# Kernel tuning notes

Hardware: AMD Instinct MI355X
Metric: run time of the kernel (lower is better)

Reference implementation:

```python
import jax, jax.numpy as jnp
import numpy as np

NEG_INF = -1e9


def setup_inputs() -> dict:
    key = jax.random.key(0)
    k1, k2, k3, k4, k5, k6 = jax.random.split(key, 6)
    B, P, N, C, H = 32, 512, 64, 9, 128
    polylines = jax.random.normal(k1, (B, P, N, C), dtype=jnp.float32)
    polylines_mask = jax.random.uniform(k2, (B, P, N)) > 0.1
    # MLP params (Linear(C,H) -> ReLU -> Linear(H,H)), torch-style init scale
    W1 = jax.random.uniform(k3, (C, H), minval=-1.0, maxval=1.0) / jnp.sqrt(C)
    b1 = jax.random.uniform(k4, (H,), minval=-1.0, maxval=1.0) / jnp.sqrt(C)
    W2 = jax.random.uniform(k5, (H, H), minval=-1.0, maxval=1.0) / jnp.sqrt(H)
    b2 = jax.random.uniform(k6, (H,), minval=-1.0, maxval=1.0) / jnp.sqrt(H)
    return {"polylines": polylines, "polylines_mask": polylines_mask,
            "W1": W1, "b1": b1, "W2": W2, "b2": b2}


def reference(polylines, polylines_mask, W1, b1, W2, b2):
    # Point MLP applied to all points (invalid ones are overwritten below,
    # identical math to the torch masked-gather version).
    h = jax.nn.relu(jnp.einsum('bpnc,ch->bpnh', polylines, W1) + b1)
    feat = jnp.einsum('bpnh,hd->bpnd', h, W2) + b2  # [B,P,N,H]
    feat = jnp.where(polylines_mask[..., None], feat, NEG_INF)
    pooled = jnp.max(feat, axis=2)  # [B,P,H]
    # Polylines with no valid points pooled to NEG_INF -> zero them out.
    any_valid = jnp.any(polylines_mask, axis=2)  # [B,P]
    return jnp.where(any_valid[..., None], pooled, 0.0)
```

## Files before the change

### kernel.cpp

```cpp
#include <hip/hip_runtime.h>


using bf16x8 = __attribute__((ext_vector_type(8))) short;
using f32x4  = __attribute__((ext_vector_type(4))) float;

#define MFMA32(A,B,C) __builtin_amdgcn_mfma_f32_16x16x32_bf16((A),(B),(C),0,0,0)

__device__ __forceinline__ unsigned short f2bf(float f) {
  union { float f; unsigned int u; } v; v.f = f;
  unsigned int r = v.u + 0x7fffu + ((v.u >> 16) & 1u);
  return (unsigned short)(r >> 16);
}

__device__ __forceinline__ unsigned int pack_bf2(float a, float b) {
  union { float f; unsigned int u; } ua, ub; ua.f = a; ub.f = b;
  return __builtin_amdgcn_perm(ub.u + 0x8000u, ua.u + 0x8000u, 0x07060302u);
}

__global__ void prep1(const float* __restrict__ W1, const float* __restrict__ W2,
                      const void* __restrict__ mask,
                      unsigned short* __restrict__ w1sw, unsigned short* __restrict__ w2sw,
                      int* __restrict__ flag) {
  int b = blockIdx.x, t = threadIdx.x;
  if (b == 0) {
    __shared__ int cnt;
    if (t == 0) cnt = 0;
    __syncthreads();
    const unsigned char* mb = (const unsigned char*)mask;
    int local = 0;
    for (int i = t * 16; i < t * 16 + 16; i++) local += (mb[i] != 0) ? 1 : 0;
    atomicAdd(&cnt, local);
    __syncthreads();
    if (t == 0) *flag = (cnt > 2800) ? 1 : 0;
  } else if (b <= 2) {
    int e = (b - 1) * 256 + t;
    int lane = e & 63, grp = e >> 6;
    int li = lane & 15, q = lane >> 4;
    int h = grp * 16 + li;
    int c0 = q * 8;
    #pragma unroll
    for (int j = 0; j < 8; j++) {
      int c = c0 + j;
      w1sw[e * 8 + j] = f2bf((c < 9) ? W1[c * 128 + h] : 0.f);
    }
  } else {
    int e = (b - 3) * 256 + t;
    if (e < 2048) {
      int lane = e & 63, grp = e >> 6;
      int wr = grp >> 4, sub = grp & 15;
      int ks = sub >> 2, td = sub & 3;
      int li = lane & 15, q = lane >> 4;
      int d = wr * 64 + td * 16 + li;
      int h0 = ks * 32 + q * 8;
      #pragma unroll
      for (int j = 0; j < 8; j++)
        w2sw[e * 8 + j] = f2bf(W2[(h0 + j) * 128 + d]);
    }
  }
}

__global__ void prep2(const void* __restrict__ mask, const int* __restrict__ flagp,
                      unsigned long long* __restrict__ bits) {
  int gid = blockIdx.x * 256 + threadIdx.x;
  int flag = *flagp;
  bool v;
  if (flag) v = ((const unsigned char*)mask)[gid] != 0;
  else      v = ((const int*)mask)[gid] != 0;
  unsigned long long bm = __ballot(v);
  if ((threadIdx.x & 63) == 0)
    bits[blockIdx.x * 4 + (threadIdx.x >> 6)] = bm;
}

__global__ __launch_bounds__(256, 4) void poly_main_k(
    const float* __restrict__ X, const void* __restrict__ mask,
    const float* __restrict__ b1g, const float* __restrict__ b2g,
    const unsigned short* __restrict__ w1sw, const unsigned short* __restrict__ w2sw,
    const int* __restrict__ flagp, const unsigned long long* __restrict__ bits,
    int use_bits, float* __restrict__ out)
{
  __shared__ __align__(16) float Xs[1152];
  __shared__ __align__(16) unsigned short Hb[128 * 136];

  const int tid  = threadIdx.x;
  const int lane = tid & 63;
  const int w    = tid >> 6;
  const int wr   = w >> 1, wc = w & 1;
  const int li   = lane & 15, q = lane >> 4;

  float mf[4];
  if (use_bits) {
    unsigned long long bm = bits[(long long)blockIdx.x * 2 + wc];
    #pragma unroll
    for (int tm = 0; tm < 4; tm++)
      mf[tm] = ((bm >> (tm * 16 + li)) & 1ull) ? 0.f : -4e9f;
  } else {
    int flag = *flagp;
    long long mb = (long long)blockIdx.x * 128 + wc * 64 + li;
    if (flag) {
      const unsigned char* mp = (const unsigned char*)mask;
      #pragma unroll
      for (int tm = 0; tm < 4; tm++) mf[tm] = mp[mb + tm * 16] ? 0.f : -4e9f;
    } else {
      const int* mp = (const int*)mask;
      #pragma unroll
      for (int tm = 0; tm < 4; tm++) mf[tm] = mp[mb + tm * 16] ? 0.f : -4e9f;
    }
  }

  {
    const f32x4* xg = (const f32x4*)(X + (long long)blockIdx.x * 1152);
    f32x4* xl = (f32x4*)Xs;
    xl[tid] = xg[tid];
    if (tid < 32) xl[tid + 256] = xg[tid + 256];
  }
  __syncthreads();

  bf16x8 bx[4];
  #pragma unroll
  for (int tm = 0; tm < 4; tm++) {
    int m = wc * 64 + tm * 16 + li;
    const float* xr = Xs + m * 9;
    union { bf16x8 v; unsigned int u[4]; } uu;
    uu.u[0] = uu.u[1] = uu.u[2] = uu.u[3] = 0u;
    if (q == 0) {
      uu.u[0] = pack_bf2(xr[0], xr[1]); uu.u[1] = pack_bf2(xr[2], xr[3]);
      uu.u[2] = pack_bf2(xr[4], xr[5]); uu.u[3] = pack_bf2(xr[6], xr[7]);
    } else if (q == 1) {
      uu.u[0] = pack_bf2(xr[8], 0.f);
    }
    bx[tm] = uu.v;
  }

  f32x4 acc1[4][4];
  #pragma unroll
  for (int a = 0; a < 4; a++)
    #pragma unroll
    for (int b = 0; b < 4; b++) acc1[a][b] = f32x4{0.f, 0.f, 0.f, 0.f};
  {
    bf16x8 a1[4];
    #pragma unroll
    for (int th = 0; th < 4; th++)
      a1[th] = *(const bf16x8*)(w1sw + ((wr * 4 + th) * 64 + lane) * 8);
    #pragma unroll
    for (int th = 0; th < 4; th++)
      #pragma unroll
      for (int tm = 0; tm < 4; tm++)
        acc1[th][tm] = MFMA32(a1[th], bx[tm], acc1[th][tm]);
  }

  #pragma unroll
  for (int th = 0; th < 4; th++) {
    f32x4 bv = *(const f32x4*)(b1g + wr * 64 + th * 16 + q * 4);
    #pragma unroll
    for (int tm = 0; tm < 4; tm++) {
      int m = wc * 64 + tm * 16 + li;
      float v0 = fmaxf(acc1[th][tm][0] + bv[0], 0.f);
      float v1 = fmaxf(acc1[th][tm][1] + bv[1], 0.f);
      float v2 = fmaxf(acc1[th][tm][2] + bv[2], 0.f);
      float v3 = fmaxf(acc1[th][tm][3] + bv[3], 0.f);
      uint2 hv;
      hv.x = pack_bf2(v0, v1);
      hv.y = pack_bf2(v2, v3);
      *(uint2*)(Hb + m * 136 + wr * 64 + th * 16 + q * 4) = hv;
    }
  }
  __syncthreads();

  f32x4 acc2[4][4];
  #pragma unroll
  for (int a = 0; a < 4; a++)
    #pragma unroll
    for (int b = 0; b < 4; b++) acc2[a][b] = f32x4{0.f, 0.f, 0.f, 0.f};
  #pragma unroll
  for (int ks = 0; ks < 4; ks++) {
    bf16x8 a2[4], bb[4];
    #pragma unroll
    for (int td = 0; td < 4; td++)
      a2[td] = *(const bf16x8*)(w2sw + (((wr * 16 + ks * 4 + td) * 64) + lane) * 8);
    #pragma unroll
    for (int tm = 0; tm < 4; tm++)
      bb[tm] = *(const bf16x8*)(Hb + (wc * 64 + tm * 16 + li) * 136 + ks * 32 + q * 8);
    #pragma unroll
    for (int td = 0; td < 4; td++)
      #pragma unroll
      for (int tm = 0; tm < 4; tm++)
        acc2[td][tm] = MFMA32(a2[td], bb[tm], acc2[td][tm]);
  }

  f32x4 pooled[4];
  #pragma unroll
  for (int td = 0; td < 4; td++) {
    f32x4 bv = *(const f32x4*)(b2g + wr * 64 + td * 16 + q * 4);
    #pragma unroll
    for (int r = 0; r < 4; r++) {
      float v0 = acc2[td][0][r] + mf[0];
      float v1 = acc2[td][1][r] + mf[1];
      float v2 = acc2[td][2][r] + mf[2];
      float v3 = acc2[td][3][r] + mf[3];
      pooled[td][r] = fmaxf(fmaxf(v0, v1), fmaxf(v2, v3)) + bv[r];
    }
  }

  __syncthreads();
  float* P = (float*)Hb;
  #pragma unroll
  for (int td = 0; td < 4; td++)
    *(f32x4*)(P + (wc * 16 + li) * 132 + wr * 64 + td * 16 + q * 4) = pooled[td];
  __syncthreads();

  {
    int p = tid >> 7, d = tid & 127;
    const float* Pp = P + p * (16 * 132) + d;
    float v = Pp[0];
    #pragma unroll
    for (int j = 1; j < 16; j++) v = fmaxf(v, Pp[j * 132]);
    if (v < -1e8f) v = 0.f;
    out[(long long)blockIdx.x * 256 + tid] = v;
  }
}

extern "C" void kernel_launch(void* const* d_in, const int* in_sizes, int n_in,
                              void* d_out, int out_size, void* d_ws, size_t ws_size,
                              hipStream_t stream) {
  const float* X    = (const float*)d_in[0];
  const void*  mask = d_in[1];
  const float* W1   = (const float*)d_in[2];
  const float* b1   = (const float*)d_in[3];
  const float* W2   = (const float*)d_in[4];
  const float* b2   = (const float*)d_in[5];
  float* out = (float*)d_out;

  unsigned short* w1sw = (unsigned short*)d_ws;
  unsigned short* w2sw = (unsigned short*)((char*)d_ws + 8192);
  int* flag            = (int*)((char*)d_ws + 40960);
  unsigned long long* bits = (unsigned long long*)((char*)d_ws + 49152);
  int use_bits = (ws_size >= (size_t)(49152 + 131072)) ? 1 : 0;

  prep1<<<11, 256, 0, stream>>>(W1, W2, mask, w1sw, w2sw, flag);
  if (use_bits) prep2<<<4096, 256, 0, stream>>>(mask, flag, bits);
  poly_main_k<<<8192, 256, 0, stream>>>(X, mask, b1, b2, w1sw, w2sw, flag, bits,
                                        use_bits, out);
}
```

Baseline: 143.1 us.

## Alias shared buffers, swizzle H tile, fold biases into accumulators, drop mask prepass

Xs, the hidden tile and the pooling buffer now share one 32KB LDS region, and the launch-bound occupancy target goes from 4 to 5 blocks. The hidden tile drops its padded stride in favour of an XOR-swizzled layout to avoid bank conflicts. Both biases now seed the MFMA accumulators, removing separate add passes, and the max reductions are vectorised. The separate mask-bitmask kernel is removed, so the main kernel reads the mask directly, saving a launch but making per-lane mask loads. The extra sync and aliasing add ordering constraints.

```diff
diff --git a/kernel.cpp b/kernel.cpp
--- a/kernel.cpp
+++ b/kernel.cpp
@@ -5,6 +5,10 @@
 using f32x4  = __attribute__((ext_vector_type(4))) float;
 
 #define MFMA32(A,B,C) __builtin_amdgcn_mfma_f32_16x16x32_bf16((A),(B),(C),0,0,0)
+
+__device__ __forceinline__ f32x4 vmax4(f32x4 a, f32x4 b) {
+  return __builtin_elementwise_max(a, b);
+}
 
 __device__ __forceinline__ unsigned short f2bf(float f) {
   union { float f; unsigned int u; } v; v.f = f;
@@ -59,27 +63,16 @@
   }
 }
 
-__global__ void prep2(const void* __restrict__ mask, const int* __restrict__ flagp,
-                      unsigned long long* __restrict__ bits) {
-  int gid = blockIdx.x * 256 + threadIdx.x;
-  int flag = *flagp;
-  bool v;
-  if (flag) v = ((const unsigned char*)mask)[gid] != 0;
-  else      v = ((const int*)mask)[gid] != 0;
-  unsigned long long bm = __ballot(v);
-  if ((threadIdx.x & 63) == 0)
-    bits[blockIdx.x * 4 + (threadIdx.x >> 6)] = bm;
-}
-
-__global__ __launch_bounds__(256, 4) void poly_main_k(
+__global__ __launch_bounds__(256, 5) void poly_main_k(
     const float* __restrict__ X, const void* __restrict__ mask,
     const float* __restrict__ b1g, const float* __restrict__ b2g,
     const unsigned short* __restrict__ w1sw, const unsigned short* __restrict__ w2sw,
-    const int* __restrict__ flagp, const unsigned long long* __restrict__ bits,
-    int use_bits, float* __restrict__ out)
+    const int* __restrict__ flagp, float* __restrict__ out)
 {
-  __shared__ __align__(16) float Xs[1152];
-  __shared__ __align__(16) unsigned short Hb[128 * 136];
+  __shared__ __align__(16) unsigned char smem[32768];
+  float*          Xs = (float*)smem;
+  unsigned short* Hb = (unsigned short*)smem;
+  float*          P  = (float*)smem;
 
   const int tid  = threadIdx.x;
   const int lane = tid & 63;
@@ -88,12 +81,7 @@
   const int li   = lane & 15, q = lane >> 4;
 
   float mf[4];
-  if (use_bits) {
-    unsigned long long bm = bits[(long long)blockIdx.x * 2 + wc];
-    #pragma unroll
-    for (int tm = 0; tm < 4; tm++)
-      mf[tm] = ((bm >> (tm * 16 + li)) & 1ull) ? 0.f : -4e9f;
-  } else {
+  {
     int flag = *flagp;
     long long mb = (long long)blockIdx.x * 128 + wc * 64 + li;
     if (flag) {
@@ -130,12 +118,15 @@
     }
     bx[tm] = uu.v;
   }
+  __syncthreads();
 
   f32x4 acc1[4][4];
   #pragma unroll
-  for (int a = 0; a < 4; a++)
-    #pragma unroll
-    for (int b = 0; b < 4; b++) acc1[a][b] = f32x4{0.f, 0.f, 0.f, 0.f};
+  for (int th = 0; th < 4; th++) {
+    f32x4 bv = *(const f32x4*)(b1g + wr * 64 + th * 16 + q * 4);
+    #pragma unroll
+    for (int tm = 0; tm < 4; tm++) acc1[th][tm] = bv;
+  }
   {
     bf16x8 a1[4];
     #pragma unroll
@@ -150,27 +141,26 @@
 
   #pragma unroll
   for (int th = 0; th < 4; th++) {
-    f32x4 bv = *(const f32x4*)(b1g + wr * 64 + th * 16 + q * 4);
     #pragma unroll
     for (int tm = 0; tm < 4; tm++) {
       int m = wc * 64 + tm * 16 + li;
-      float v0 = fmaxf(acc1[th][tm][0] + bv[0], 0.f);
-      float v1 = fmaxf(acc1[th][tm][1] + bv[1], 0.f);
-      float v2 = fmaxf(acc1[th][tm][2] + bv[2], 0.f);
-      float v3 = fmaxf(acc1[th][tm][3] + bv[3], 0.f);
+      f32x4 v = vmax4(acc1[th][tm], f32x4{0.f, 0.f, 0.f, 0.f});
       uint2 hv;
-      hv.x = pack_bf2(v0, v1);
-      hv.y = pack_bf2(v2, v3);
-      *(uint2*)(Hb + m * 136 + wr * 64 + th * 16 + q * 4) = hv;
+      hv.x = pack_bf2(v[0], v[1]);
+      hv.y = pack_bf2(v[2], v[3]);
+      int chunk = (wr * 8 + th * 2 + (q >> 1)) ^ li;
+      *(uint2*)(Hb + m * 128 + chunk * 8 + (q & 1) * 4) = hv;
     }
   }
   __syncthreads();
 
   f32x4 acc2[4][4];
   #pragma unroll
-  for (int a = 0; a < 4; a++)
-    #pragma unroll
-    for (int b = 0; b < 4; b++) acc2[a][b] = f32x4{0.f, 0.f, 0.f, 0.f};
+  for (int td = 0; td < 4; td++) {
+    f32x4 bv = *(const f32x4*)(b2g + wr * 64 + td * 16 + q * 4);
+    #pragma unroll
+    for (int tm = 0; tm < 4; tm++) acc2[td][tm] = bv;
+  }
   #pragma unroll
   for (int ks = 0; ks < 4; ks++) {
     bf16x8 a2[4], bb[4];
@@ -178,8 +168,11 @@
     for (int td = 0; td < 4; td++)
       a2[td] = *(const bf16x8*)(w2sw + (((wr * 16 + ks * 4 + td) * 64) + lane) * 8);
     #pragma unroll
-    for (int tm = 0; tm < 4; tm++)
-      bb[tm] = *(const bf16x8*)(Hb + (wc * 64 + tm * 16 + li) * 136 + ks * 32 + q * 8);
+    for (int tm = 0; tm < 4; tm++) {
+      int m = wc * 64 + tm * 16 + li;
+      int chunk = (ks * 4 + q) ^ li;
+      bb[tm] = *(const bf16x8*)(Hb + m * 128 + chunk * 8);
+    }
     #pragma unroll
     for (int td = 0; td < 4; td++)
       #pragma unroll
@@ -190,19 +183,14 @@
   f32x4 pooled[4];
   #pragma unroll
   for (int td = 0; td < 4; td++) {
-    f32x4 bv = *(const f32x4*)(b2g + wr * 64 + td * 16 + q * 4);
-    #pragma unroll
-    for (int r = 0; r < 4; r++) {
-      float v0 = acc2[td][0][r] + mf[0];
-      float v1 = acc2[td][1][r] + mf[1];
-      float v2 = acc2[td][2][r] + mf[2];
-      float v3 = acc2[td][3][r] + mf[3];
-      pooled[td][r] = fmaxf(fmaxf(v0, v1), fmaxf(v2, v3)) + bv[r];
-    }
-  }
-
-  __syncthreads();
-  float* P = (float*)Hb;
+    f32x4 v = acc2[td][0] + mf[0];
+    v = vmax4(v, acc2[td][1] + mf[1]);
+    v = vmax4(v, acc2[td][2] + mf[2]);
+    v = vmax4(v, acc2[td][3] + mf[3]);
+    pooled[td] = v;
+  }
+
+  __syncthreads();
   #pragma unroll
   for (int td = 0; td < 4; td++)
     *(f32x4*)(P + (wc * 16 + li) * 132 + wr * 64 + td * 16 + q * 4) = pooled[td];
@@ -233,11 +221,7 @@
   unsigned short* w1sw = (unsigned short*)d_ws;
   unsigned short* w2sw = (unsigned short*)((char*)d_ws + 8192);
   int* flag            = (int*)((char*)d_ws + 40960);
-  unsigned long long* bits = (unsigned long long*)((char*)d_ws + 49152);
-  int use_bits = (ws_size >= (size_t)(49152 + 131072)) ? 1 : 0;
 
   prep1<<<11, 256, 0, stream>>>(W1, W2, mask, w1sw, w2sw, flag);
-  if (use_bits) prep2<<<4096, 256, 0, stream>>>(mask, flag, bits);
-  poly_main_k<<<8192, 256, 0, stream>>>(X, mask, b1, b2, w1sw, w2sw, flag, bits,
-                                        use_bits, out);
-}
+  poly_main_k<<<8192, 256, 0, stream>>>(X, mask, b1, b2, w1sw, w2sw, flag, out);
+}
```

Measured after the change: 180.5 us. 1.26x slower.
